# Kernel tuning notes

Measured on AMD Instinct MI355X. Metric: run time of the kernel, lower is better.

Reference implementation:

```python
import jax, jax.numpy as jnp
import numpy as np

MAX_ITER = 10
TAU = 1.0


def setup_inputs() -> dict:
    key = jax.random.key(0)
    k1, k2, k3 = jax.random.split(key, 3)
    B, R, C = 64, 1024, 1024
    s = jax.random.normal(k1, (B, R, C), dtype=jnp.float32)
    # nrows <= ncols per batch => no transposed_batch branch in the original
    nrows = jax.random.randint(k2, (B,), 128, 512).astype(jnp.int32)
    ncols = jax.random.randint(k3, (B,), 512, C + 1).astype(jnp.int32)
    return {"s": s, "nrows": nrows, "ncols": ncols}


def _masked_lse(x, mask, axis):
    """logsumexp over `axis` restricted to mask==True; finite-safe everywhere.
    Equivalent to torch.logsumexp after writing -inf into masked-out entries,
    but keeps all values finite so grads are clean."""
    neg = jnp.asarray(-1e30, x.dtype)
    m = jax.lax.stop_gradient(jnp.max(jnp.where(mask, x, neg), axis=axis, keepdims=True))
    e = jnp.where(mask, jnp.exp(jnp.where(mask, x, m) - m), jnp.zeros((), x.dtype))
    sum_e = jnp.sum(e, axis=axis, keepdims=True)
    any_m = jnp.any(mask, axis=axis, keepdims=True)
    return m + jnp.log(jnp.where(any_m, sum_e, jnp.ones((), x.dtype)))


def _sinkhorn(s, nrows, ncols):
    B, R, C = s.shape
    row_mask = (jnp.arange(R)[None, :] < nrows[:, None])[:, :, None]  # [B,R,1]
    col_mask = (jnp.arange(C)[None, :] < ncols[:, None])[:, None, :]  # [B,1,C]
    valid = row_mask & col_mask                                        # [B,R,C]
    log_s = s / TAU
    # Alternating row/col normalization in log space. In the original, entries
    # outside [nrows,ncols] are set to -inf and ignored by logsumexp; here we
    # keep them finite and mask inside the logsumexp, which is the same math
    # on the valid region, and we zero the invalid region at the end (exp(-inf)=0).
    for i in range(MAX_ITER):
        if i % 2 == 0:  # row normalization
            lse = _masked_lse(log_s, valid, axis=2)          # [B,R,1]
            log_s = log_s - jnp.where(row_mask, lse, 0.0)
        else:           # col normalization
            lse = _masked_lse(log_s, valid, axis=1)          # [B,1,C]
            log_s = log_s - jnp.where(col_mask, lse, 0.0)
    return jnp.where(valid, jnp.exp(log_s), jnp.zeros((), s.dtype))


def reference(s, nrows, ncols):
    return _sinkhorn(s, nrows, ncols)
```

## Files before the change

kernel.cpp:

```cpp
#include <hip/hip_runtime.h>
#include <hip/hip_fp16.h>


#define B_DIM 64
#define RCH 32

__device__ __forceinline__ float fast_rcp(float x) {
#if __has_builtin(__builtin_amdgcn_rcpf)
    return __builtin_amdgcn_rcpf(x);
#else
    return 1.0f / x;
#endif
}

__device__ __forceinline__ float wave_sum(float x) {
    #pragma unroll
    for (int off = 1; off < 64; off <<= 1) x += __shfl_xor(x, off);
    return x;
}

__device__ __forceinline__ void phase2_col(
    const __half* __restrict__ e_lds,
    const float* __restrict__ a_lds, int b, int nc, int t,
    float* __restrict__ cs_cur)
{
    const int c0 = t << 1;
    if (c0 >= nc) return;
    float s0 = 0.f, s1 = 0.f;
    #pragma unroll
    for (int rr = 0; rr < RCH; ++rr) {
        const float2 f = __half22float2(
            *reinterpret_cast<const __half2*>(e_lds + (rr << 10) + c0));
        const float av = a_lds[rr];
        s0 = fmaf(f.x, av, s0);
        s1 = fmaf(f.y, av, s1);
    }
    if (s0 != 0.f) atomicAdd(cs_cur + (b << 10) + c0, s0);
    if (s1 != 0.f) atomicAdd(cs_cur + (b << 10) + c0 + 1, s1);
}

__device__ __forceinline__ void decode_pair_bid(int bid, int& b, int& rc) {
    const int xcd = bid & 7;
    const int j = bid >> 3;
    rc = j & 15;
    b = (xcd << 3) | (j >> 4);
}

__global__ __launch_bounds__(512) void pair_first(
    const float* __restrict__ s, const int* __restrict__ nrows,
    const int* __restrict__ ncols, __half* __restrict__ E,
    float* __restrict__ a, float* __restrict__ cs_cur,
    float* __restrict__ cs_next)
{
    int b, rc;
    decode_pair_bid(blockIdx.x, b, rc);
    const int t = threadIdx.x;
    if (t < 64) cs_next[(b << 10) + (rc << 6) + t] = 0.f;

    const int nr = nrows[b];
    const int r0 = rc << 5;
    if (r0 >= nr) return;
    const int nc = ncols[b];

    __shared__ __half e_lds[RCH * 1024];
    __shared__ float a_lds[RCH];

    const int wave = t >> 6;
    const int lane = t & 63;
    const int cbase = lane << 4;
    const bool cOK = cbase < nc;

    #pragma unroll 1
    for (int k = 0; k < 4; ++k) {
        const int rr = (wave << 2) + k;
        const int r = r0 + rr;
        float sum = 0.f;
        __half2 h[8];
        if (r < nr && cOK) {
            const float* __restrict__ srow =
                s + ((size_t)b << 20) + ((size_t)r << 10) + cbase;
            float e[16];
            #pragma unroll
            for (int q = 0; q < 4; ++q) {
                const float4 x = *reinterpret_cast<const float4*>(srow + (q << 2));
                e[4 * q + 0] = __expf(x.x); e[4 * q + 1] = __expf(x.y);
                e[4 * q + 2] = __expf(x.z); e[4 * q + 3] = __expf(x.w);
            }
            #pragma unroll
            for (int j = 0; j < 16; ++j)
                if (cbase + j >= nc) e[j] = 0.f;
            #pragma unroll
            for (int q = 0; q < 8; ++q)
                h[q] = __floats2half2_rn(e[2 * q], e[2 * q + 1]);
            __half* __restrict__ erow =
                E + ((size_t)b << 19) + ((size_t)r << 10) + cbase;
            *reinterpret_cast<float4*>(erow)     = *reinterpret_cast<const float4*>(&h[0]);
            *reinterpret_cast<float4*>(erow + 8) = *reinterpret_cast<const float4*>(&h[4]);
            #pragma unroll
            for (int j = 0; j < 16; ++j) sum += e[j];
        } else {
            #pragma unroll
            for (int q = 0; q < 8; ++q) h[q] = __floats2half2_rn(0.f, 0.f);
        }
        __half* dst = e_lds + (rr << 10) + cbase;
        *reinterpret_cast<float4*>(dst)     = *reinterpret_cast<const float4*>(&h[0]);
        *reinterpret_cast<float4*>(dst + 8) = *reinterpret_cast<const float4*>(&h[4]);
        sum = wave_sum(sum);
        if (lane == 0) a_lds[rr] = (r < nr) ? 1.0f / sum : 0.f;
    }
    __syncthreads();
    if (t < RCH) a[(b << 9) + r0 + t] = a_lds[t];

    phase2_col(e_lds, a_lds, b, nc, t, cs_cur);
}

__global__ __launch_bounds__(512) void pair_mid(
    const __half* __restrict__ E, const int* __restrict__ nrows,
    const int* __restrict__ ncols, const float* __restrict__ cs_prev,
    float* __restrict__ a, float* __restrict__ cs_cur,
    float* __restrict__ cs_next)
{
    int b, rc;
    decode_pair_bid(blockIdx.x, b, rc);
    const int t = threadIdx.x;
    if (t < 64) cs_next[(b << 10) + (rc << 6) + t] = 0.f;

    const int nr = nrows[b];
    const int r0 = rc << 5;
    if (r0 >= nr) return;
    const int nc = ncols[b];

    __shared__ __half e_lds[RCH * 1024];
    __shared__ float a_lds[RCH];

    const int wave = t >> 6;
    const int lane = t & 63;
    const int cbase = lane << 4;
    const bool cOK = cbase < nc;

    float w[16];
    if (cOK) {
        const float* __restrict__ csp = cs_prev + (b << 10) + cbase;
        #pragma unroll
        for (int q = 0; q < 4; ++q) {
            const float4 c4 = *reinterpret_cast<const float4*>(csp + (q << 2));
            w[4 * q + 0] = (cbase + 4 * q + 0 < nc) ? fast_rcp(c4.x) : 0.f;
            w[4 * q + 1] = (cbase + 4 * q + 1 < nc) ? fast_rcp(c4.y) : 0.f;
            w[4 * q + 2] = (cbase + 4 * q + 2 < nc) ? fast_rcp(c4.z) : 0.f;
            w[4 * q + 3] = (cbase + 4 * q + 3 < nc) ? fast_rcp(c4.w) : 0.f;
        }
    }

    #pragma unroll 1
    for (int k = 0; k < 4; ++k) {
        const int rr = (wave << 2) + k;
        const int r = r0 + rr;
        float s0 = 0.f, s1 = 0.f;
        float4 p0, p1;
        if (r < nr && cOK) {
            const __half* __restrict__ erow =
                E + ((size_t)b << 19) + ((size_t)r << 10) + cbase;
            p0 = *reinterpret_cast<const float4*>(erow);
            p1 = *reinterpret_cast<const float4*>(erow + 8);
            const __half2* h0 = reinterpret_cast<const __half2*>(&p0);
            const __half2* h1 = reinterpret_cast<const __half2*>(&p1);
            #pragma unroll
            for (int q = 0; q < 4; ++q) {
                const float2 f = __half22float2(h0[q]);
                s0 = fmaf(f.x, w[2 * q], s0);
                s1 = fmaf(f.y, w[2 * q + 1], s1);
            }
            #pragma unroll
            for (int q = 0; q < 4; ++q) {
                const float2 f = __half22float2(h1[q]);
                s0 = fmaf(f.x, w[8 + 2 * q], s0);
                s1 = fmaf(f.y, w[8 + 2 * q + 1], s1);
            }
        } else {
            p0 = make_float4(0.f, 0.f, 0.f, 0.f);
            p1 = p0;
        }
        __half* dst = e_lds + (rr << 10) + cbase;
        *reinterpret_cast<float4*>(dst)     = p0;
        *reinterpret_cast<float4*>(dst + 8) = p1;
        const float sum = wave_sum(s0 + s1);
        if (lane == 0) a_lds[rr] = (r < nr) ? 1.0f / sum : 0.f;
    }
    __syncthreads();
    if (t < RCH) a[(b << 9) + r0 + t] = a_lds[t];

    phase2_col(e_lds, a_lds, b, nc, t, cs_cur);
}

__global__ __launch_bounds__(256) void out_step_f(
    const __half* __restrict__ E, const int* __restrict__ nrows,
    const int* __restrict__ ncols, const float* __restrict__ a,
    const float* __restrict__ cs, float* __restrict__ out)
{
    const int bid = blockIdx.x;
    const int xcd = bid & 7;
    const int j = bid >> 3;
    const int r = j & 1023;
    const int b = (xcd << 3) | (j >> 10);
    const int c0 = threadIdx.x << 2;

    const int nr = nrows[b];
    const int nc = ncols[b];
    float4 o = make_float4(0.f, 0.f, 0.f, 0.f);
    if (r < nr && c0 < nc) {
        const float ar = a[(b << 9) + r];
        float2 pk = *reinterpret_cast<const float2*>(
            E + ((size_t)b << 19) + ((size_t)r << 10) + c0);
        const float2 f01 = __half22float2(reinterpret_cast<const __half2*>(&pk)[0]);
        const float2 f23 = __half22float2(reinterpret_cast<const __half2*>(&pk)[1]);
        const float4 c4 = *reinterpret_cast<const float4*>(cs + (b << 10) + c0);
        o.x = f01.x * ar * fast_rcp(c4.x);
        o.y = (c0 + 1 < nc) ? f01.y * ar * fast_rcp(c4.y) : 0.f;
        o.z = (c0 + 2 < nc) ? f23.x * ar * fast_rcp(c4.z) : 0.f;
        o.w = (c0 + 3 < nc) ? f23.y * ar * fast_rcp(c4.w) : 0.f;
    }
    *reinterpret_cast<float4*>(out + ((size_t)b << 20) + ((size_t)r << 10) + c0) = o;
}


__global__ __launch_bounds__(256) void row_step_lg(
    const float* __restrict__ s, const int* __restrict__ nrows,
    const int* __restrict__ ncols, const float* __restrict__ vlog,
    const int use_v, float* __restrict__ u)
{
    const int b = blockIdx.y, r = blockIdx.x;
    const int nr = nrows[b];
    if (r >= nr) return;
    const int nc = ncols[b];
    const int t = threadIdx.x, c0 = t << 2;
    float sum = 0.f;
    if (c0 < nc) {
        const float4 x = reinterpret_cast<const float4*>(
            s + ((size_t)b << 20) + ((size_t)r << 10))[t];
        float4 vv = make_float4(0.f, 0.f, 0.f, 0.f);
        if (use_v) vv = reinterpret_cast<const float4*>(vlog + ((size_t)b << 10))[t];
        sum  = (c0 + 0 < nc) ? __expf(x.x - vv.x) : 0.f;
        sum += (c0 + 1 < nc) ? __expf(x.y - vv.y) : 0.f;
        sum += (c0 + 2 < nc) ? __expf(x.z - vv.z) : 0.f;
        sum += (c0 + 3 < nc) ? __expf(x.w - vv.w) : 0.f;
    }
    #pragma unroll
    for (int off = 1; off < 64; off <<= 1) sum += __shfl_xor(sum, off);
    __shared__ float ss[4];
    if ((t & 63) == 0) ss[t >> 6] = sum;
    __syncthreads();
    if (t == 0) u[((size_t)b << 9) + r] = __logf(ss[0] + ss[1] + ss[2] + ss[3]);
}

__global__ __launch_bounds__(256) void col_step_lg(
    const float* __restrict__ s, const int* __restrict__ nrows,
    const int* __restrict__ ncols, const float* __restrict__ u,
    float* __restrict__ partial)
{
    const int b = blockIdx.z, rc = blockIdx.y;
    const int nr = nrows[b];
    const int r0 = rc << 6;
    if (r0 >= nr) return;
    const int nc = ncols[b];
    const int c = (blockIdx.x << 8) + threadIdx.x;
    float sum = 0.f;
    if (c < nc) {
        const int rend = min(r0 + 64, nr);
        const float* __restrict__ sb = s + ((size_t)b << 20) + c;
        const float* __restrict__ ub = u + ((size_t)b << 9);
        float s0 = 0.f, s1 = 0.f, s2 = 0.f, s3 = 0.f;
        int r = r0;
        for (; r + 4 <= rend; r += 4) {
            s0 += __expf(sb[(size_t)(r + 0) << 10] - ub[r + 0]);
            s1 += __expf(sb[(size_t)(r + 1) << 10] - ub[r + 1]);
            s2 += __expf(sb[(size_t)(r + 2) << 10] - ub[r + 2]);
            s3 += __expf(sb[(size_t)(r + 3) << 10] - ub[r + 3]);
        }
        for (; r < rend; ++r) s0 += __expf(sb[(size_t)r << 10] - ub[r]);
        sum = (s0 + s1) + (s2 + s3);
    }
    partial[(((size_t)b << 3) + rc) << 10 | c] = sum;
}

__global__ __launch_bounds__(256) void col_fin_lg(
    const int* __restrict__ nrows, const float* __restrict__ partial,
    float* __restrict__ vlog)
{
    const int idx = (blockIdx.x << 8) + threadIdx.x;
    const int b = idx >> 10;
    const int nch = (nrows[b] + 63) >> 6;
    const float* __restrict__ p = partial + ((size_t)(b << 3) << 10) + (idx & 1023);
    float sum = 0.f;
    for (int k = 0; k < nch; ++k) sum += p[(size_t)k << 10];
    vlog[idx] = (sum > 0.f) ? __logf(sum) : 0.f;
}

__global__ __launch_bounds__(256) void out_step_lg(
    const float* __restrict__ s, const int* __restrict__ nrows,
    const int* __restrict__ ncols, const float* __restrict__ u,
    const float* __restrict__ vlog, float* __restrict__ out)
{
    const size_t total4 = (size_t)B_DIM * 1024 * 1024 / 4;
    float4* out4 = reinterpret_cast<float4*>(out);
    const float4* s4 = reinterpret_cast<const float4*>(s);
    for (size_t i = (size_t)blockIdx.x * blockDim.x + threadIdx.x; i < total4;
         i += (size_t)gridDim.x * blockDim.x) {
        const int b = (int)(i >> 18);
        const int rem = (int)(i & 262143);
        const int r = rem >> 8;
        const int c0 = (rem & 255) << 2;
        const int nr = nrows[b], nc = ncols[b];
        float4 o;
        if (r >= nr || c0 >= nc) {
            o = make_float4(0.f, 0.f, 0.f, 0.f);
        } else {
            float4 x = s4[i];
            const float ur = u[((size_t)b << 9) + r];
            const float* vb = vlog + ((size_t)b << 10);
            o.x = (c0 + 0 < nc) ? __expf(x.x - ur - vb[c0 + 0]) : 0.f;
            o.y = (c0 + 1 < nc) ? __expf(x.y - ur - vb[c0 + 1]) : 0.f;
            o.z = (c0 + 2 < nc) ? __expf(x.z - ur - vb[c0 + 2]) : 0.f;
            o.w = (c0 + 3 < nc) ? __expf(x.w - ur - vb[c0 + 3]) : 0.f;
        }
        out4[i] = o;
    }
}


extern "C" void kernel_launch(void* const* d_in, const int* in_sizes, int n_in,
                              void* d_out, int out_size, void* d_ws, size_t ws_size,
                              hipStream_t stream) {
    const float* s = (const float*)d_in[0];
    const int* nrows = (const int*)d_in[1];
    const int* ncols = (const int*)d_in[2];
    float* out = (float*)d_out;

    const size_t E_BYTES = (size_t)B_DIM * 512 * 1024 * 2;
    const size_t CS_ELEMS = (size_t)B_DIM * 1024;
    const size_t NEED = E_BYTES + (size_t)B_DIM * 512 * 4 + 3 * CS_ELEMS * 4;

    if (ws_size >= NEED) {
        __half* E = (__half*)d_ws;
        float* a = (float*)((char*)d_ws + E_BYTES);
        float* cs0 = a + B_DIM * 512;
        float* cs1 = cs0 + CS_ELEMS;
        float* cs2 = cs1 + CS_ELEMS;

        hipMemsetAsync(cs0, 0, CS_ELEMS * sizeof(float), stream);

        const int nblk = 16 * B_DIM;
        pair_first<<<nblk, 512, 0, stream>>>(s, nrows, ncols, E, a, cs0, cs1);
        pair_mid<<<nblk, 512, 0, stream>>>(E, nrows, ncols, cs0, a, cs1, cs2);
        pair_mid<<<nblk, 512, 0, stream>>>(E, nrows, ncols, cs1, a, cs2, cs0);
        pair_mid<<<nblk, 512, 0, stream>>>(E, nrows, ncols, cs2, a, cs0, cs1);
        pair_mid<<<nblk, 512, 0, stream>>>(E, nrows, ncols, cs0, a, cs1, cs2);
        out_step_f<<<65536, 256, 0, stream>>>(E, nrows, ncols, a, cs1, out);
    } else {
        float* u = (float*)d_ws;
        float* vlog = u + (size_t)B_DIM * 512;
        float* partial = vlog + (size_t)B_DIM * 1024;
        const dim3 rowGrid(512, B_DIM);
        const dim3 colGrid(4, 8, B_DIM);
        for (int it = 0; it < 5; ++it) {
            row_step_lg<<<rowGrid, 256, 0, stream>>>(s, nrows, ncols, vlog, it, u);
            col_step_lg<<<colGrid, 256, 0, stream>>>(s, nrows, ncols, u, partial);
            col_fin_lg<<<256, 256, 0, stream>>>(nrows, partial, vlog);
        }
        out_step_lg<<<4096, 256, 0, stream>>>(s, nrows, ncols, u, vlog, out);
    }
}
```

Measured before the change: 162.9 us.

## Fuse all Sinkhorn iterations into one cooperative kernel keeping E in registers

Replaces the chain of per-iteration kernels, which round-trip an fp16 exp matrix through global memory, with a single cooperative kernel. Each block holds its 64 rows of exp(s) for one batch in registers as fp16 and runs the row and column normalizations in place. Column sums are reduced through LDS and global atomics, with grid.sync between phases. This removes repeated E reads and writes plus launch overhead, at the cost of heavy register pressure, grid-wide barriers and a fallback path if the cooperative launch fails.

Result: slower. 576.9 us (+254.1%).

```diff
diff --git a/kernel.cpp b/kernel.cpp
--- a/kernel.cpp
+++ b/kernel.cpp
@@ -1,9 +1,10 @@
 #include <hip/hip_runtime.h>
 #include <hip/hip_fp16.h>
-
+#include <hip/hip_cooperative_groups.h>
+
+namespace cg = cooperative_groups;
 
 #define B_DIM 64
-#define RCH 32
 
 __device__ __forceinline__ float fast_rcp(float x) {
 #if __has_builtin(__builtin_amdgcn_rcpf)
@@ -19,10 +20,217 @@
     return x;
 }
 
+
+__global__ __launch_bounds__(512, 4) void sinkhorn_coop(
+    const float* __restrict__ s, const int* __restrict__ nrows,
+    const int* __restrict__ ncols, float* __restrict__ cs0,
+    float* __restrict__ cs1, float* __restrict__ cs2,
+    float* __restrict__ out)
+{
+    cg::grid_group grid = cg::this_grid();
+    __shared__ float cls[8 * 1024];
+
+    const int g = blockIdx.x;
+    const int b = g >> 3;
+    const int half = g & 7;
+    const int t = threadIdx.x;
+    const int w = t >> 6;
+    const int l = t & 63;
+    const int c4 = l << 2;
+    const int nr = nrows[b];
+    const int nc = ncols[b];
+    const int rbase = (half << 6) + (w << 2);
+
+    float4 eA[2][4], eB[2][4];
+    float aR[2][4];
+
+    if (t < 128) cs1[(b << 10) + (half << 7) + t] = 0.f;
+
+    #pragma unroll
+    for (int q = 0; q < 2; ++q) {
+        #pragma unroll
+        for (int rw = 0; rw < 4; ++rw) {
+            const int r = rbase + (q << 5) + rw;
+            float e[16];
+            if (r < nr) {
+                const float* __restrict__ srow =
+                    s + ((size_t)b << 20) + ((size_t)r << 10);
+                const float4 x0 = *reinterpret_cast<const float4*>(srow + c4);
+                const float4 x1 = *reinterpret_cast<const float4*>(srow + 256 + c4);
+                e[0] = __expf(x0.x); e[1] = __expf(x0.y);
+                e[2] = __expf(x0.z); e[3] = __expf(x0.w);
+                e[4] = __expf(x1.x); e[5] = __expf(x1.y);
+                e[6] = __expf(x1.z); e[7] = __expf(x1.w);
+                #pragma unroll
+                for (int j = 2; j < 4; ++j) {
+                    const int c = (j << 8) + c4;
+                    if (c < nc) {
+                        const float4 x = *reinterpret_cast<const float4*>(srow + c);
+                        e[j*4+0] = __expf(x.x);
+                        e[j*4+1] = (c + 1 < nc) ? __expf(x.y) : 0.f;
+                        e[j*4+2] = (c + 2 < nc) ? __expf(x.z) : 0.f;
+                        e[j*4+3] = (c + 3 < nc) ? __expf(x.w) : 0.f;
+                    } else {
+                        e[j*4+0] = 0.f; e[j*4+1] = 0.f;
+                        e[j*4+2] = 0.f; e[j*4+3] = 0.f;
+                    }
+                }
+            } else {
+                #pragma unroll
+                for (int i = 0; i < 16; ++i) e[i] = 0.f;
+            }
+            __half2 h[8];
+            #pragma unroll
+            for (int k = 0; k < 8; ++k)
+                h[k] = __floats2half2_rn(e[2*k], e[2*k+1]);
+            eA[q][rw] = *reinterpret_cast<const float4*>(&h[0]);
+            eB[q][rw] = *reinterpret_cast<const float4*>(&h[4]);
+            float acc = 0.f;
+            #pragma unroll
+            for (int i = 0; i < 16; ++i) acc += e[i];
+            acc = wave_sum(acc);
+            aR[q][rw] = (r < nr) ? fast_rcp(acc) : 0.f;
+        }
+    }
+
+    auto col_phase = [&](float* __restrict__ cscur) {
+        float4 p[4];
+        p[0] = make_float4(0.f, 0.f, 0.f, 0.f); p[1] = p[0];
+        p[2] = p[0]; p[3] = p[0];
+        #pragma unroll
+        for (int q = 0; q < 2; ++q) {
+            #pragma unroll
+            for (int rw = 0; rw < 4; ++rw) {
+                const float av = aR[q][rw];
+                const __half2* hA = reinterpret_cast<const __half2*>(&eA[q][rw]);
+                const __half2* hB = reinterpret_cast<const __half2*>(&eB[q][rw]);
+                float2 f;
+                f = __half22float2(hA[0]); p[0].x = fmaf(f.x, av, p[0].x); p[0].y = fmaf(f.y, av, p[0].y);
+                f = __half22float2(hA[1]); p[0].z = fmaf(f.x, av, p[0].z); p[0].w = fmaf(f.y, av, p[0].w);
+                f = __half22float2(hA[2]); p[1].x = fmaf(f.x, av, p[1].x); p[1].y = fmaf(f.y, av, p[1].y);
+                f = __half22float2(hA[3]); p[1].z = fmaf(f.x, av, p[1].z); p[1].w = fmaf(f.y, av, p[1].w);
+                f = __half22float2(hB[0]); p[2].x = fmaf(f.x, av, p[2].x); p[2].y = fmaf(f.y, av, p[2].y);
+                f = __half22float2(hB[1]); p[2].z = fmaf(f.x, av, p[2].z); p[2].w = fmaf(f.y, av, p[2].w);
+                f = __half22float2(hB[2]); p[3].x = fmaf(f.x, av, p[3].x); p[3].y = fmaf(f.y, av, p[3].y);
+                f = __half22float2(hB[3]); p[3].z = fmaf(f.x, av, p[3].z); p[3].w = fmaf(f.y, av, p[3].w);
+            }
+        }
+        #pragma unroll
+        for (int j = 0; j < 4; ++j)
+            *reinterpret_cast<float4*>(cls + (w << 10) + (j << 8) + c4) = p[j];
+        __syncthreads();
+        float* __restrict__ cur = cscur + (b << 10);
+        #pragma unroll
+        for (int hh = 0; hh < 2; ++hh) {
+            const int c = t + (hh << 9);
+            float v = 0.f;
+            #pragma unroll
+            for (int ww = 0; ww < 8; ++ww) v += cls[(ww << 10) + c];
+            if (v != 0.f) atomicAdd(cur + c, v);
+        }
+    };
+
+    auto row_phase = [&](const float* __restrict__ csprev) {
+        float4 wv[4];
+        const float* __restrict__ csb = csprev + (b << 10);
+        #pragma unroll
+        for (int j = 0; j < 4; ++j) {
+            const int c = (j << 8) + c4;
+            const float4 v = *reinterpret_cast<const float4*>(csb + c);
+            wv[j].x = (c + 0 < nc) ? fast_rcp(v.x) : 0.f;
+            wv[j].y = (c + 1 < nc) ? fast_rcp(v.y) : 0.f;
+            wv[j].z = (c + 2 < nc) ? fast_rcp(v.z) : 0.f;
+            wv[j].w = (c + 3 < nc) ? fast_rcp(v.w) : 0.f;
+        }
+        #pragma unroll
+        for (int q = 0; q < 2; ++q) {
+            #pragma unroll
+            for (int rw = 0; rw < 4; ++rw) {
+                const int r = rbase + (q << 5) + rw;
+                const __half2* hA = reinterpret_cast<const __half2*>(&eA[q][rw]);
+                const __half2* hB = reinterpret_cast<const __half2*>(&eB[q][rw]);
+                float2 f;
+                float a0, a1;
+                f = __half22float2(hA[0]); a0 = f.x * wv[0].x;            a1 = f.y * wv[0].y;
+                f = __half22float2(hA[1]); a0 = fmaf(f.x, wv[0].z, a0);   a1 = fmaf(f.y, wv[0].w, a1);
+                f = __half22float2(hA[2]); a0 = fmaf(f.x, wv[1].x, a0);   a1 = fmaf(f.y, wv[1].y, a1);
+                f = __half22float2(hA[3]); a0 = fmaf(f.x, wv[1].z, a0);   a1 = fmaf(f.y, wv[1].w, a1);
+                f = __half22float2(hB[0]); a0 = fmaf(f.x, wv[2].x, a0);   a1 = fmaf(f.y, wv[2].y, a1);
+                f = __half22float2(hB[1]); a0 = fmaf(f.x, wv[2].z, a0);   a1 = fmaf(f.y, wv[2].w, a1);
+                f = __half22float2(hB[2]); a0 = fmaf(f.x, wv[3].x, a0);   a1 = fmaf(f.y, wv[3].y, a1);
+                f = __half22float2(hB[3]); a0 = fmaf(f.x, wv[3].z, a0);   a1 = fmaf(f.y, wv[3].w, a1);
+                const float sum = wave_sum(a0 + a1);
+                aR[q][rw] = (r < nr) ? fast_rcp(sum) : 0.f;
+            }
+        }
+    };
+
+    col_phase(cs0);  grid.sync();
+    if (t < 128) cs2[(b << 10) + (half << 7) + t] = 0.f;
+    row_phase(cs0);  col_phase(cs1);  grid.sync();
+    if (t < 128) cs0[(b << 10) + (half << 7) + t] = 0.f;
+    row_phase(cs1);  col_phase(cs2);  grid.sync();
+    if (t < 128) cs1[(b << 10) + (half << 7) + t] = 0.f;
+    row_phase(cs2);  col_phase(cs0);  grid.sync();
+    row_phase(cs0);  col_phase(cs1);  grid.sync();
+
+    {
+        float4 wv[4];
+        const float* __restrict__ csb = cs1 + (b << 10);
+        #pragma unroll
+        for (int j = 0; j < 4; ++j) {
+            const int c = (j << 8) + c4;
+            const float4 v = *reinterpret_cast<const float4*>(csb + c);
+            wv[j].x = (c + 0 < nc) ? fast_rcp(v.x) : 0.f;
+            wv[j].y = (c + 1 < nc) ? fast_rcp(v.y) : 0.f;
+            wv[j].z = (c + 2 < nc) ? fast_rcp(v.z) : 0.f;
+            wv[j].w = (c + 3 < nc) ? fast_rcp(v.w) : 0.f;
+        }
+        #pragma unroll
+        for (int q = 0; q < 2; ++q) {
+            #pragma unroll
+            for (int rw = 0; rw < 4; ++rw) {
+                const int r = rbase + (q << 5) + rw;
+                const float av = aR[q][rw];
+                float* __restrict__ orow =
+                    out + ((size_t)b << 20) + ((size_t)r << 10);
+                const __half2* hA = reinterpret_cast<const __half2*>(&eA[q][rw]);
+                const __half2* hB = reinterpret_cast<const __half2*>(&eB[q][rw]);
+                float2 fa, fb;
+                float4 o;
+                fa = __half22float2(hA[0]); fb = __half22float2(hA[1]);
+                o = make_float4(fa.x*av*wv[0].x, fa.y*av*wv[0].y,
+                                fb.x*av*wv[0].z, fb.y*av*wv[0].w);
+                *reinterpret_cast<float4*>(orow + c4) = o;
+                fa = __half22float2(hA[2]); fb = __half22float2(hA[3]);
+                o = make_float4(fa.x*av*wv[1].x, fa.y*av*wv[1].y,
+                                fb.x*av*wv[1].z, fb.y*av*wv[1].w);
+                *reinterpret_cast<float4*>(orow + 256 + c4) = o;
+                fa = __half22float2(hB[0]); fb = __half22float2(hB[1]);
+                o = make_float4(fa.x*av*wv[2].x, fa.y*av*wv[2].y,
+                                fb.x*av*wv[2].z, fb.y*av*wv[2].w);
+                *reinterpret_cast<float4*>(orow + 512 + c4) = o;
+                fa = __half22float2(hB[2]); fb = __half22float2(hB[3]);
+                o = make_float4(fa.x*av*wv[3].x, fa.y*av*wv[3].y,
+                                fb.x*av*wv[3].z, fb.y*av*wv[3].w);
+                *reinterpret_cast<float4*>(orow + 768 + c4) = o;
+            }
+        }
+        const float4 z = make_float4(0.f, 0.f, 0.f, 0.f);
+        float4* __restrict__ zbase = reinterpret_cast<float4*>(
+            out + ((size_t)b << 20) + ((size_t)(512 + (half << 6)) << 10));
+        #pragma unroll 4
+        for (int idx = t; idx < 64 * 256; idx += 512)
+            zbase[idx] = z;
+    }
+}
+
+
+#define RCH 32
+
 __device__ __forceinline__ void phase2_col(
-    const __half* __restrict__ e_lds,
-    const float* __restrict__ a_lds, int b, int nc, int t,
-    float* __restrict__ cs_cur)
+    const __half* __restrict__ e_lds, const float* __restrict__ a_lds,
+    int b, int nc, int t, float* __restrict__ cs_cur)
 {
     const int c0 = t << 1;
     if (c0 >= nc) return;
@@ -83,15 +291,15 @@
             #pragma unroll
             for (int q = 0; q < 4; ++q) {
                 const float4 x = *reinterpret_cast<const float4*>(srow + (q << 2));
-                e[4 * q + 0] = __expf(x.x); e[4 * q + 1] = __expf(x.y);
-                e[4 * q + 2] = __expf(x.z); e[4 * q + 3] = __expf(x.w);
+                e[4*q+0] = __expf(x.x); e[4*q+1] = __expf(x.y);
+                e[4*q+2] = __expf(x.z); e[4*q+3] = __expf(x.w);
             }
             #pragma unroll
             for (int j = 0; j < 16; ++j)
                 if (cbase + j >= nc) e[j] = 0.f;
             #pragma unroll
             for (int q = 0; q < 8; ++q)
-                h[q] = __floats2half2_rn(e[2 * q], e[2 * q + 1]);
+                h[q] = __floats2half2_rn(e[2*q], e[2*q+1]);
             __half* __restrict__ erow =
                 E + ((size_t)b << 19) + ((size_t)r << 10) + cbase;
             *reinterpret_cast<float4*>(erow)     = *reinterpret_cast<const float4*>(&h[0]);
@@ -138,16 +346,16 @@
     const int cbase = lane << 4;
     const bool cOK = cbase < nc;
 
-    float w[16];
+    float wgt[16];
     if (cOK) {
         const float* __restrict__ csp = cs_prev + (b << 10) + cbase;
         #pragma unroll
         for (int q = 0; q < 4; ++q) {
-            const float4 c4 = *reinterpret_cast<const float4*>(csp + (q << 2));
-            w[4 * q + 0] = (cbase + 4 * q + 0 < nc) ? fast_rcp(c4.x) : 0.f;
-            w[4 * q + 1] = (cbase + 4 * q + 1 < nc) ? fast_rcp(c4.y) : 0.f;
-            w[4 * q + 2] = (cbase + 4 * q + 2 < nc) ? fast_rcp(c4.z) : 0.f;
-            w[4 * q + 3] = (cbase + 4 * q + 3 < nc) ? fast_rcp(c4.w) : 0.f;
+            const float4 c4v = *reinterpret_cast<const float4*>(csp + (q << 2));
+            wgt[4*q+0] = (cbase + 4*q + 0 < nc) ? fast_rcp(c4v.x) : 0.f;
+            wgt[4*q+1] = (cbase + 4*q + 1 < nc) ? fast_rcp(c4v.y) : 0.f;
+            wgt[4*q+2] = (cbase + 4*q + 2 < nc) ? fast_rcp(c4v.z) : 0.f;
+            wgt[4*q+3] = (cbase + 4*q + 3 < nc) ? fast_rcp(c4v.w) : 0.f;
         }
     }
 
@@ -167,14 +375,14 @@
             #pragma unroll
             for (int q = 0; q < 4; ++q) {
                 const float2 f = __half22float2(h0[q]);
-                s0 = fmaf(f.x, w[2 * q], s0);
-                s1 = fmaf(f.y, w[2 * q + 1], s1);
+                s0 = fmaf(f.x, wgt[2*q], s0);
+                s1 = fmaf(f.y, wgt[2*q+1], s1);
             }
             #pragma unroll
             for (int q = 0; q < 4; ++q) {
                 const float2 f = __half22float2(h1[q]);
-                s0 = fmaf(f.x, w[8 + 2 * q], s0);
-                s1 = fmaf(f.y, w[8 + 2 * q + 1], s1);
+                s0 = fmaf(f.x, wgt[8+2*q], s0);
+                s1 = fmaf(f.y, wgt[8+2*q+1], s1);
             }
         } else {
             p0 = make_float4(0.f, 0.f, 0.f, 0.f);
@@ -213,117 +421,13 @@
             E + ((size_t)b << 19) + ((size_t)r << 10) + c0);
         const float2 f01 = __half22float2(reinterpret_cast<const __half2*>(&pk)[0]);
         const float2 f23 = __half22float2(reinterpret_cast<const __half2*>(&pk)[1]);
-        const float4 c4 = *reinterpret_cast<const float4*>(cs + (b << 10) + c0);
-        o.x = f01.x * ar * fast_rcp(c4.x);
-        o.y = (c0 + 1 < nc) ? f01.y * ar * fast_rcp(c4.y) : 0.f;
-        o.z = (c0 + 2 < nc) ? f23.x * ar * fast_rcp(c4.z) : 0.f;
-        o.w = (c0 + 3 < nc) ? f23.y * ar * fast_rcp(c4.w) : 0.f;
+        const float4 c4v = *reinterpret_cast<const float4*>(cs + (b << 10) + c0);
+        o.x = f01.x * ar * fast_rcp(c4v.x);
+        o.y = (c0 + 1 < nc) ? f01.y * ar * fast_rcp(c4v.y) : 0.f;
+        o.z = (c0 + 2 < nc) ? f23.x * ar * fast_rcp(c4v.z) : 0.f;
+        o.w = (c0 + 3 < nc) ? f23.y * ar * fast_rcp(c4v.w) : 0.f;
     }
     *reinterpret_cast<float4*>(out + ((size_t)b << 20) + ((size_t)r << 10) + c0) = o;
-}
-
-
-__global__ __launch_bounds__(256) void row_step_lg(
-    const float* __restrict__ s, const int* __restrict__ nrows,
-    const int* __restrict__ ncols, const float* __restrict__ vlog,
-    const int use_v, float* __restrict__ u)
-{
-    const int b = blockIdx.y, r = blockIdx.x;
-    const int nr = nrows[b];
-    if (r >= nr) return;
-    const int nc = ncols[b];
-    const int t = threadIdx.x, c0 = t << 2;
-    float sum = 0.f;
-    if (c0 < nc) {
-        const float4 x = reinterpret_cast<const float4*>(
-            s + ((size_t)b << 20) + ((size_t)r << 10))[t];
-        float4 vv = make_float4(0.f, 0.f, 0.f, 0.f);
-        if (use_v) vv = reinterpret_cast<const float4*>(vlog + ((size_t)b << 10))[t];
-        sum  = (c0 + 0 < nc) ? __expf(x.x - vv.x) : 0.f;
-        sum += (c0 + 1 < nc) ? __expf(x.y - vv.y) : 0.f;
-        sum += (c0 + 2 < nc) ? __expf(x.z - vv.z) : 0.f;
-        sum += (c0 + 3 < nc) ? __expf(x.w - vv.w) : 0.f;
-    }
-    #pragma unroll
-    for (int off = 1; off < 64; off <<= 1) sum += __shfl_xor(sum, off);
-    __shared__ float ss[4];
-    if ((t & 63) == 0) ss[t >> 6] = sum;
-    __syncthreads();
-    if (t == 0) u[((size_t)b << 9) + r] = __logf(ss[0] + ss[1] + ss[2] + ss[3]);
-}
-
-__global__ __launch_bounds__(256) void col_step_lg(
-    const float* __restrict__ s, const int* __restrict__ nrows,
-    const int* __restrict__ ncols, const float* __restrict__ u,
-    float* __restrict__ partial)
-{
-    const int b = blockIdx.z, rc = blockIdx.y;
-    const int nr = nrows[b];
-    const int r0 = rc << 6;
-    if (r0 >= nr) return;
-    const int nc = ncols[b];
-    const int c = (blockIdx.x << 8) + threadIdx.x;
-    float sum = 0.f;
-    if (c < nc) {
-        const int rend = min(r0 + 64, nr);
-        const float* __restrict__ sb = s + ((size_t)b << 20) + c;
-        const float* __restrict__ ub = u + ((size_t)b << 9);
-        float s0 = 0.f, s1 = 0.f, s2 = 0.f, s3 = 0.f;
-        int r = r0;
-        for (; r + 4 <= rend; r += 4) {
-            s0 += __expf(sb[(size_t)(r + 0) << 10] - ub[r + 0]);
-            s1 += __expf(sb[(size_t)(r + 1) << 10] - ub[r + 1]);
-            s2 += __expf(sb[(size_t)(r + 2) << 10] - ub[r + 2]);
-            s3 += __expf(sb[(size_t)(r + 3) << 10] - ub[r + 3]);
-        }
-        for (; r < rend; ++r) s0 += __expf(sb[(size_t)r << 10] - ub[r]);
-        sum = (s0 + s1) + (s2 + s3);
-    }
-    partial[(((size_t)b << 3) + rc) << 10 | c] = sum;
-}
-
-__global__ __launch_bounds__(256) void col_fin_lg(
-    const int* __restrict__ nrows, const float* __restrict__ partial,
-    float* __restrict__ vlog)
-{
-    const int idx = (blockIdx.x << 8) + threadIdx.x;
-    const int b = idx >> 10;
-    const int nch = (nrows[b] + 63) >> 6;
-    const float* __restrict__ p = partial + ((size_t)(b << 3) << 10) + (idx & 1023);
-    float sum = 0.f;
-    for (int k = 0; k < nch; ++k) sum += p[(size_t)k << 10];
-    vlog[idx] = (sum > 0.f) ? __logf(sum) : 0.f;
-}
-
-__global__ __launch_bounds__(256) void out_step_lg(
-    const float* __restrict__ s, const int* __restrict__ nrows,
-    const int* __restrict__ ncols, const float* __restrict__ u,
-    const float* __restrict__ vlog, float* __restrict__ out)
-{
-    const size_t total4 = (size_t)B_DIM * 1024 * 1024 / 4;
-    float4* out4 = reinterpret_cast<float4*>(out);
-    const float4* s4 = reinterpret_cast<const float4*>(s);
-    for (size_t i = (size_t)blockIdx.x * blockDim.x + threadIdx.x; i < total4;
-         i += (size_t)gridDim.x * blockDim.x) {
-        const int b = (int)(i >> 18);
-        const int rem = (int)(i & 262143);
-        const int r = rem >> 8;
-        const int c0 = (rem & 255) << 2;
-        const int nr = nrows[b], nc = ncols[b];
-        float4 o;
-        if (r >= nr || c0 >= nc) {
-            o = make_float4(0.f, 0.f, 0.f, 0.f);
-        } else {
-            float4 x = s4[i];
-            const float ur = u[((size_t)b << 9) + r];
-            const float* vb = vlog + ((size_t)b << 10);
-            o.x = (c0 + 0 < nc) ? __expf(x.x - ur - vb[c0 + 0]) : 0.f;
-            o.y = (c0 + 1 < nc) ? __expf(x.y - ur - vb[c0 + 1]) : 0.f;
-            o.z = (c0 + 2 < nc) ? __expf(x.z - ur - vb[c0 + 2]) : 0.f;
-            o.w = (c0 + 3 < nc) ? __expf(x.w - ur - vb[c0 + 3]) : 0.f;
-        }
-        out4[i] = o;
-    }
 }
 
 
@@ -335,16 +439,33 @@
     const int* ncols = (const int*)d_in[2];
     float* out = (float*)d_out;
 
+    const size_t CS_ELEMS = (size_t)B_DIM * 1024;
+
+    bool coop_done = false;
+    if (ws_size >= 3 * CS_ELEMS * sizeof(float)) {
+        float* cs0 = (float*)d_ws;
+        float* cs1 = cs0 + CS_ELEMS;
+        float* cs2 = cs1 + CS_ELEMS;
+        hipMemsetAsync(cs0, 0, CS_ELEMS * sizeof(float), stream);
+        void* args[] = {(void*)&s, (void*)&nrows, (void*)&ncols,
+                        (void*)&cs0, (void*)&cs1, (void*)&cs2, (void*)&out};
+        hipError_t err = hipLaunchCooperativeKernel(
+            reinterpret_cast<const void*>(sinkhorn_coop),
+            dim3(512), dim3(512), args, 0, stream);
+        coop_done = (err == hipSuccess);
+        if (!coop_done) (void)hipGetLastError();
+    }
+    if (coop_done) return;
+
     const size_t E_BYTES = (size_t)B_DIM * 512 * 1024 * 2;
-    const size_t CS_ELEMS = (size_t)B_DIM * 1024;
-    const size_t NEED = E_BYTES + (size_t)B_DIM * 512 * 4 + 3 * CS_ELEMS * 4;
-
-    if (ws_size >= NEED) {
+    float* cs0f;
+    {
         __half* E = (__half*)d_ws;
         float* a = (float*)((char*)d_ws + E_BYTES);
         float* cs0 = a + B_DIM * 512;
         float* cs1 = cs0 + CS_ELEMS;
         float* cs2 = cs1 + CS_ELEMS;
+        cs0f = cs0;
 
         hipMemsetAsync(cs0, 0, CS_ELEMS * sizeof(float), stream);
 
@@ -355,17 +476,6 @@
         pair_mid<<<nblk, 512, 0, stream>>>(E, nrows, ncols, cs2, a, cs0, cs1);
         pair_mid<<<nblk, 512, 0, stream>>>(E, nrows, ncols, cs0, a, cs1, cs2);
         out_step_f<<<65536, 256, 0, stream>>>(E, nrows, ncols, a, cs1, out);
-    } else {
-        float* u = (float*)d_ws;
-        float* vlog = u + (size_t)B_DIM * 512;
-        float* partial = vlog + (size_t)B_DIM * 1024;
-        const dim3 rowGrid(512, B_DIM);
-        const dim3 colGrid(4, 8, B_DIM);
-        for (int it = 0; it < 5; ++it) {
-            row_step_lg<<<rowGrid, 256, 0, stream>>>(s, nrows, ncols, vlog, it, u);
-            col_step_lg<<<colGrid, 256, 0, stream>>>(s, nrows, ncols, u, partial);
-            col_fin_lg<<<256, 256, 0, stream>>>(nrows, partial, vlog);
-        }
-        out_step_lg<<<4096, 256, 0, stream>>>(s, nrows, ncols, u, vlog, out);
-    }
-}
+    }
+    (void)cs0f;
+}
```
